# Optimization experiments

Hardware: AMD Instinct MI355X
Metric: run time of the kernel (lower is better)

## Reference

```python
import math
import jax, jax.numpy as jnp
import numpy as np

B, DIN, DOUT = 16384, 512, 512
LATERAL_K = 3
K_WTA = max(1, int(DOUT * 0.25))


def _build_L_mask(dout: int, k: int) -> np.ndarray:
    m = np.zeros((dout, dout), dtype=np.float32)
    for j in range(dout):
        nb = []
        for off in range(1, k + 1):
            if j - off >= 0:
                nb.append(j - off)
            if j + off < dout:
                nb.append(j + off)
        for n in nb[:k]:
            m[j, n] = 1.0
    return m


def _kwta_mask(x):
    # top-k winner-take-all mask along last dim (ties resolved like torch.topk)
    _, idx = jax.lax.top_k(x, K_WTA)
    rows = jnp.arange(x.shape[0])[:, None]
    return jnp.zeros_like(x).at[rows, idx].set(1.0)


def _phi(x, mask):
    return jax.nn.gelu(x, approximate=False) * mask


def _phi_deriv(x, mask):
    cdf = 0.5 * (1.0 + jax.lax.erf(x / math.sqrt(2.0)))
    pdf = jnp.exp(-0.5 * x * x) / math.sqrt(2.0 * math.pi)
    return (cdf + x * pdf) * mask


def _clip_update(d, max_norm):
    n = jnp.linalg.norm(d)  # global norm over the whole tensor, as in torch
    return jnp.where(n > max_norm, d * (max_norm / (n + 1e-8)), d)


def setup_inputs() -> dict:
    key = jax.random.key(0)
    ks = jax.random.split(key, 8)
    k_v = math.sqrt(1.0 / DIN)
    k_w = math.sqrt(1.0 / DOUT)
    return {
        "bottom_up": jax.random.normal(ks[0], (B, DIN), jnp.float32),
        "td_target": jax.random.normal(ks[1], (B, DOUT), jnp.float32) * 0.5,
        "x": jax.random.normal(ks[2], (B, DOUT), jnp.float32) * 0.5,
        "V": jax.random.uniform(ks[3], (DIN, DOUT), jnp.float32, -k_v, k_v),
        "b_in": jnp.full((DOUT,), -5.0, jnp.float32),
        "W_snap": jax.random.uniform(ks[4], (DOUT, DIN), jnp.float32, -k_w, k_w),
        "b_out_snap": jnp.zeros((DIN,), jnp.float32),
        "L": jax.random.uniform(ks[5], (DOUT, DOUT), jnp.float32, -0.1, 0.1),
        "L_mask": jnp.asarray(_build_L_mask(DOUT, LATERAL_K)),
        "step_i": 2,
    }


def reference(bottom_up, td_target, x, V, b_in, W_snap, b_out_snap, L, L_mask, step_i):
    tau, eta_x, lambda_act = 0.5, 0.8, 1e-6
    mask = _kwta_mask(x)
    phi_x = _phi(x, mask)                                     # [B, DOUT]
    prediction = phi_x @ W_snap + b_out_snap                  # [B, DIN]
    error = jax.lax.stop_gradient(bottom_up - prediction)     # detached in torch
    feedback_drive = (error @ W_snap.T) * _phi_deriv(x, mask)
    forward_drive = bottom_up @ V + b_in                      # [B, DOUT]
    recognition_drive = forward_drive - x                     # recognition_weight=1.0
    top_down_drive = 3.0 * (td_target - x)
    lateral_drive = phi_x @ (L * L_mask)
    state_grad = (feedback_drive + recognition_drive + top_down_drive
                  + 0.3 * lateral_drive - lambda_act * jnp.sign(x))
    eta = eta_x / (1.0 + 0.1 * step_i)
    dx = _clip_update(tau * eta * state_grad, 1.0)
    return jnp.clip(x + dx, -5.0, 5.0)
```

## Files before the change

kernel.cpp:

```cpp
#include <hip/hip_runtime.h>
#include <hip/hip_bf16.h>
#include <cstdint>


#define DEV static __device__ __forceinline__

typedef __attribute__((ext_vector_type(8))) short short8;
typedef __attribute__((ext_vector_type(4))) float f32x4;

static constexpr int BATCH = 16384;
static constexpr int D = 512;

DEV unsigned short f2bf(float f) {
  unsigned u = __float_as_uint(f);
  return (unsigned short)((u + 0x7FFFu + ((u >> 16) & 1u)) >> 16);
}
DEV float bf2f(unsigned short h) { return __uint_as_float(((unsigned)h) << 16); }

DEV float wsumf(float v) { for (int o = 32; o; o >>= 1) v += __shfl_xor(v, o, 64); return v; }

DEV void gload16(const void* g, void* l) {
  __builtin_amdgcn_global_load_lds((const __attribute__((address_space(1))) void*)g,
                                   (__attribute__((address_space(3))) void*)l, 16, 0, 0);
}

DEV void load8(const float* rowp, int lane, float v[8]) {
  const float4* q = (const float4*)rowp;
  float4 a = q[lane * 2], b = q[lane * 2 + 1];
  v[0] = a.x; v[1] = a.y; v[2] = a.z; v[3] = a.w;
  v[4] = b.x; v[5] = b.y; v[6] = b.z; v[7] = b.w;
}

__global__ __launch_bounds__(256) void prep_k(
    const float* __restrict__ W, const float* __restrict__ V,
    const float* __restrict__ L, const float* __restrict__ Lm,
    unsigned short* __restrict__ Wbt, unsigned short* __restrict__ Wb2,
    unsigned short* __restrict__ Vbt, float* __restrict__ Mc7,
    float* __restrict__ ssq)
{
  int idx = blockIdx.x * 256 + threadIdx.x;
  int n = idx >> 9, k = idx & 511;
  Wbt[idx] = f2bf(W[k * D + n]);
  Wb2[idx] = f2bf(W[idx]);
  Vbt[idx] = f2bf(V[k * D + n]);
  if (idx < 7 * D) {
    int t = idx >> 9, nn = idx & 511;
    int j = nn - 3 + t;
    float v = 0.f;
    if (j >= 0 && j < D && j != nn) v = L[j * D + nn] * Lm[j * D + nn];
    Mc7[idx] = v;
  }
  if (idx == 0) *ssq = 0.f;
}

__global__ __launch_bounds__(256) void kwta_k(
    const float* __restrict__ x, const float* __restrict__ td,
    const float* __restrict__ bu, const float* __restrict__ b_in,
    const float* __restrict__ Mc7,
    unsigned short* __restrict__ phi16, unsigned short* __restrict__ pd16,
    unsigned short* __restrict__ base16, unsigned short* __restrict__ bu16)
{
  __shared__ float pbuf[4][D];
  const int tid = threadIdx.x, lane = tid & 63, wv = tid >> 6;
  const int row = blockIdx.x * 4 + wv;
  const size_t rbase = (size_t)row * D;

  float xv[8];
  load8(x + rbase, lane, xv);
  unsigned key[8];
  #pragma unroll
  for (int s = 0; s < 8; ++s) {
    unsigned u = __float_as_uint(xv[s]);
    key[s] = (u & 0x80000000u) ? ~u : (u | 0x80000000u);
  }
  unsigned T = 0u;
  for (int bit = 31; bit >= 0; --bit) {
    unsigned cand = T | (1u << bit);
    int c = 0;
    #pragma unroll
    for (int s = 0; s < 8; ++s) c += (int)__popcll(__ballot(key[s] >= cand));
    T = (c >= 128) ? cand : T;
  }
  int cg = 0;
  unsigned long long em[8];
  #pragma unroll
  for (int s = 0; s < 8; ++s) {
    cg += (int)__popcll(__ballot(key[s] > T));
    em[s] = __ballot(key[s] == T);
  }
  const int rneed = 128 - cg;
  const unsigned long long lower = (1ull << lane) - 1ull;
  int run = 0;
  #pragma unroll
  for (int s = 0; s < 8; ++s) run += (int)__popcll(em[s] & lower);

  float phiv[8], pdv[8];
  float* pb = pbuf[wv];
  #pragma unroll
  for (int s = 0; s < 8; ++s) {
    bool sel = key[s] > T;
    if (key[s] == T) { sel = (run < rneed); ++run; }
    float v = xv[s];
    float cdf = 0.5f * (1.0f + erff(v * 0.7071067811865476f));
    float ph = sel ? v * cdf : 0.0f;
    float pd = sel ? (cdf + v * 0.3989422804014327f * __expf(-0.5f * v * v)) : 0.0f;
    phiv[s] = ph; pdv[s] = pd;
    pb[(s << 6) | lane] = ph;
  }
  __syncthreads();

  float tdv[8], buv[8];
  load8(td + rbase, lane, tdv);
  load8(bu + rbase, lane, buv);

  float lat[8] = {0.f, 0.f, 0.f, 0.f, 0.f, 0.f, 0.f, 0.f};
  #pragma unroll
  for (int t = 0; t < 7; ++t) {
    const float4* mq = (const float4*)(Mc7 + t * D + lane * 8);
    float4 m0 = mq[0], m1 = mq[1];
    float mm[8] = {m0.x, m0.y, m0.z, m0.w, m1.x, m1.y, m1.z, m1.w};
    #pragma unroll
    for (int s = 0; s < 8; ++s) {
      int j = lane * 8 + s - 3 + t;
      int jc = j < 0 ? 0 : (j > D - 1 ? D - 1 : j);
      lat[s] += mm[s] * pb[((jc & 7) << 6) | (jc >> 3)];
    }
  }

  short8 o_phi, o_pd, o_base, o_bu;
  #pragma unroll
  for (int s = 0; s < 8; ++s) {
    int n = lane * 8 + s;
    float v = xv[s];
    float sgn = (v > 0.f) ? 1.f : ((v < 0.f) ? -1.f : 0.f);
    float bs = b_in[n] + 3.f * tdv[s] - 4.f * v + 0.3f * lat[s] - 1e-6f * sgn;
    o_phi[s] = (short)f2bf(phiv[s]);
    o_pd[s]  = (short)f2bf(pdv[s]);
    o_base[s]= (short)f2bf(bs);
    o_bu[s]  = (short)f2bf(buv[s]);
  }
  *(short8*)(phi16 + rbase + lane * 8) = o_phi;
  *(short8*)(pd16  + rbase + lane * 8) = o_pd;
  *(short8*)(base16+ rbase + lane * 8) = o_base;
  *(short8*)(bu16  + rbase + lane * 8) = o_bu;
}

template<int MODE>
__global__ __launch_bounds__(256) void gemm_k(
    const unsigned short* __restrict__ A,
    const unsigned short* __restrict__ Bt,
    const float* __restrict__ f32b,
    const unsigned short* __restrict__ b16a,
    const unsigned short* __restrict__ b16b,
    unsigned short* __restrict__ out16,
    float* __restrict__ outf,
    float* __restrict__ ssq,
    const int* __restrict__ stepi)
{
  constexpr int K = 512;
  __shared__ __align__(16) unsigned short As[128 * 32];
  __shared__ __align__(16) unsigned short Bs[128 * 32];
  const int tid = threadIdx.x;
  const int lane = tid & 63, w = tid >> 6;
  const int m0 = (blockIdx.x >> 2) * 128, n0 = (blockIdx.x & 3) * 128;
  const int qr = (w >> 1) * 64, qc = (w & 1) * 64;
  const int lr = lane & 15, g = lane >> 4;

  f32x4 acc[4][4];
  #pragma unroll
  for (int m = 0; m < 4; ++m)
    #pragma unroll
    for (int n = 0; n < 4; ++n) acc[m][n] = (f32x4){0.f, 0.f, 0.f, 0.f};

  const unsigned short* Abase = A + (size_t)m0 * K;
  const unsigned short* Bbase = Bt + (size_t)n0 * K;

  for (int kt = 0; kt < K; kt += 32) {
    #pragma unroll
    for (int p = 0; p < 2; ++p) {
      int ch = tid + p * 256;
      int row = ch >> 2, kc = (ch & 3) * 8;
      gload16(Abase + (size_t)row * K + kt + kc, As + (size_t)(w * 64 + p * 256) * 8);
      gload16(Bbase + (size_t)row * K + kt + kc, Bs + (size_t)(w * 64 + p * 256) * 8);
    }
    __syncthreads();
    short8 af[4], bfr[4];
    #pragma unroll
    for (int m = 0; m < 4; ++m) af[m]  = *(const short8*)(As + (qr + 16 * m + lr) * 32 + 8 * g);
    #pragma unroll
    for (int n = 0; n < 4; ++n) bfr[n] = *(const short8*)(Bs + (qc + 16 * n + lr) * 32 + 8 * g);
    #pragma unroll
    for (int m = 0; m < 4; ++m)
      #pragma unroll
      for (int n = 0; n < 4; ++n)
        acc[m][n] = __builtin_amdgcn_mfma_f32_16x16x32_bf16(af[m], bfr[n], acc[m][n], 0, 0, 0);
    __syncthreads();
  }

  float tau_eta = 0.f, lssq = 0.f;
  if constexpr (MODE == 3) tau_eta = 0.5f * 0.8f / (1.0f + 0.1f * (float)stepi[0]);
  #pragma unroll
  for (int m = 0; m < 4; ++m) {
    #pragma unroll
    for (int n = 0; n < 4; ++n) {
      #pragma unroll
      for (int r = 0; r < 4; ++r) {
        int row = m0 + qr + 16 * m + 4 * g + r;
        int col = n0 + qc + 16 * n + lr;
        size_t idx = (size_t)row * D + col;
        float v = acc[m][n][r];
        if constexpr (MODE == 1) {
          out16[idx] = f2bf(bf2f(b16a[idx]) - (v + f32b[col]));
        } else if constexpr (MODE == 2) {
          out16[idx] = f2bf(v * bf2f(b16a[idx]));
        } else {
          float dv = tau_eta * (v + bf2f(b16a[idx]) + bf2f(b16b[idx]));
          outf[idx] = dv;
          lssq += dv * dv;
        }
      }
    }
  }
  if constexpr (MODE == 3) {
    lssq = wsumf(lssq);
    if (lane == 0) atomicAdd(ssq, lssq);
  }
}

__global__ __launch_bounds__(256) void final_k(const float* __restrict__ x,
                                               float* __restrict__ d,
                                               const float* __restrict__ ssq)
{
  float nrm = sqrtf(*ssq);
  float s = nrm > 1.0f ? 1.0f / (nrm + 1e-8f) : 1.0f;
  int i = blockIdx.x * 256 + threadIdx.x;
  const float4* xq = (const float4*)x;
  float4* dq = (float4*)d;
  float4 xv = xq[i], dv = dq[i];
  float4 o;
  o.x = fminf(fmaxf(xv.x + s * dv.x, -5.f), 5.f);
  o.y = fminf(fmaxf(xv.y + s * dv.y, -5.f), 5.f);
  o.z = fminf(fmaxf(xv.z + s * dv.z, -5.f), 5.f);
  o.w = fminf(fmaxf(xv.w + s * dv.w, -5.f), 5.f);
  dq[i] = o;
}

extern "C" void kernel_launch(void* const* d_in, const int* in_sizes, int n_in,
                              void* d_out, int out_size, void* d_ws, size_t ws_size,
                              hipStream_t stream) {
  const float* bu    = (const float*)d_in[0];
  const float* td    = (const float*)d_in[1];
  const float* x     = (const float*)d_in[2];
  const float* V     = (const float*)d_in[3];
  const float* b_in  = (const float*)d_in[4];
  const float* W     = (const float*)d_in[5];
  const float* bout  = (const float*)d_in[6];
  const float* L     = (const float*)d_in[7];
  const float* Lm    = (const float*)d_in[8];
  const int*   stepi = (const int*)d_in[9];
  float* dout = (float*)d_out;

  char* p = (char*)d_ws;
  size_t off = 0;
  auto take = [&](size_t bytes) -> void* {
    void* r = (void*)(p + off);
    off += (bytes + 255) & ~(size_t)255;
    return r;
  };
  float* ssq            = (float*)take(4);
  unsigned short* Wbt   = (unsigned short*)take((size_t)D * D * 2);
  unsigned short* Wb2   = (unsigned short*)take((size_t)D * D * 2);
  unsigned short* Vbt   = (unsigned short*)take((size_t)D * D * 2);
  float* Mc7            = (float*)take((size_t)7 * D * 4);
  const size_t bd = (size_t)BATCH * D * 2;
  unsigned short* phi16 = (unsigned short*)take(bd);
  unsigned short* bu16  = (unsigned short*)take(bd);
  unsigned short* pd16  = (unsigned short*)take(bd);
  unsigned short* bse16 = (unsigned short*)take(bd);
  unsigned short* err16 = (unsigned short*)take(bd);
  unsigned short* fb16  = phi16;

  prep_k<<<(D * D) / 256, 256, 0, stream>>>(W, V, L, Lm, Wbt, Wb2, Vbt, Mc7, ssq);
  kwta_k<<<BATCH / 4, 256, 0, stream>>>(x, td, bu, b_in, Mc7, phi16, pd16, bse16, bu16);
  gemm_k<1><<<(BATCH / 128) * (D / 128), 256, 0, stream>>>(
      phi16, Wbt, bout, bu16, nullptr, err16, nullptr, nullptr, nullptr);
  gemm_k<2><<<(BATCH / 128) * (D / 128), 256, 0, stream>>>(
      err16, Wb2, nullptr, pd16, nullptr, fb16, nullptr, nullptr, nullptr);
  gemm_k<3><<<(BATCH / 128) * (D / 128), 256, 0, stream>>>(
      bu16, Vbt, nullptr, fb16, bse16, nullptr, dout, ssq, stepi);
  final_k<<<(BATCH * D / 4) / 256, 256, 0, stream>>>(x, dout, ssq);
}
```

Measured before the change: 263.4 us.

## Double-buffer GEMM tiles, swizzle blocks, approximate erf, early-exit top-k, bf16 dx

Measured after the change: 278.7 us. 5.8% more time.

```diff
diff --git a/kernel.cpp b/kernel.cpp
--- a/kernel.cpp
+++ b/kernel.cpp
@@ -74,36 +74,56 @@
     key[s] = (u & 0x80000000u) ? ~u : (u | 0x80000000u);
   }
   unsigned T = 0u;
+  bool exact = false;
   for (int bit = 31; bit >= 0; --bit) {
     unsigned cand = T | (1u << bit);
     int c = 0;
     #pragma unroll
     for (int s = 0; s < 8; ++s) c += (int)__popcll(__ballot(key[s] >= cand));
-    T = (c >= 128) ? cand : T;
-  }
-  int cg = 0;
-  unsigned long long em[8];
-  #pragma unroll
-  for (int s = 0; s < 8; ++s) {
-    cg += (int)__popcll(__ballot(key[s] > T));
-    em[s] = __ballot(key[s] == T);
-  }
-  const int rneed = 128 - cg;
-  const unsigned long long lower = (1ull << lane) - 1ull;
-  int run = 0;
-  #pragma unroll
-  for (int s = 0; s < 8; ++s) run += (int)__popcll(em[s] & lower);
+    if (c == 128) { T = cand; exact = true; break; }
+    if (c > 128) T = cand;
+  }
+
+  bool selv[8];
+  if (exact) {
+    #pragma unroll
+    for (int s = 0; s < 8; ++s) selv[s] = (key[s] >= T);
+  } else {
+    int cg = 0;
+    unsigned long long em[8];
+    #pragma unroll
+    for (int s = 0; s < 8; ++s) {
+      cg += (int)__popcll(__ballot(key[s] > T));
+      em[s] = __ballot(key[s] == T);
+    }
+    const int rneed = 128 - cg;
+    const unsigned long long lower = (1ull << lane) - 1ull;
+    int run = 0;
+    #pragma unroll
+    for (int s = 0; s < 8; ++s) run += (int)__popcll(em[s] & lower);
+    #pragma unroll
+    for (int s = 0; s < 8; ++s) {
+      bool sel = key[s] > T;
+      if (key[s] == T) { sel = (run < rneed); ++run; }
+      selv[s] = sel;
+    }
+  }
 
   float phiv[8], pdv[8];
   float* pb = pbuf[wv];
   #pragma unroll
   for (int s = 0; s < 8; ++s) {
-    bool sel = key[s] > T;
-    if (key[s] == T) { sel = (run < rneed); ++run; }
     float v = xv[s];
-    float cdf = 0.5f * (1.0f + erff(v * 0.7071067811865476f));
-    float ph = sel ? v * cdf : 0.0f;
-    float pd = sel ? (cdf + v * 0.3989422804014327f * __expf(-0.5f * v * v)) : 0.0f;
+    float e  = __expf(-0.5f * v * v);
+    float az = fabsf(v) * 0.7071067811865476f;
+    float t  = __builtin_amdgcn_rcpf(1.0f + 0.3275911f * az);
+    float p  = 0.254829592f + t * (-0.284496736f + t * (1.421413741f +
+               t * (-1.453152027f + t * 1.061405429f)));
+    float erfa = 1.0f - p * t * e;
+    float erfs = (v < 0.f) ? -erfa : erfa;
+    float cdf = 0.5f * (1.0f + erfs);
+    float ph = selv[s] ? v * cdf : 0.0f;
+    float pd = selv[s] ? (cdf + v * 0.3989422804014327f * e) : 0.0f;
     phiv[s] = ph; pdv[s] = pd;
     pb[(s << 6) | lane] = ph;
   }
@@ -153,16 +173,17 @@
     const unsigned short* __restrict__ b16a,
     const unsigned short* __restrict__ b16b,
     unsigned short* __restrict__ out16,
-    float* __restrict__ outf,
     float* __restrict__ ssq,
     const int* __restrict__ stepi)
 {
   constexpr int K = 512;
-  __shared__ __align__(16) unsigned short As[128 * 32];
-  __shared__ __align__(16) unsigned short Bs[128 * 32];
+  constexpr int NT = K / 32;
+  __shared__ __align__(16) unsigned short As[2][128 * 32];
+  __shared__ __align__(16) unsigned short Bs[2][128 * 32];
   const int tid = threadIdx.x;
   const int lane = tid & 63, w = tid >> 6;
-  const int m0 = (blockIdx.x >> 2) * 128, n0 = (blockIdx.x & 3) * 128;
+  const int lid = (blockIdx.x & 7) * 64 + (blockIdx.x >> 3);
+  const int m0 = (lid >> 2) * 128, n0 = (lid & 3) * 128;
   const int qr = (w >> 1) * 64, qc = (w & 1) * 64;
   const int lr = lane & 15, g = lane >> 4;
 
@@ -175,20 +196,27 @@
   const unsigned short* Abase = A + (size_t)m0 * K;
   const unsigned short* Bbase = Bt + (size_t)n0 * K;
 
-  for (int kt = 0; kt < K; kt += 32) {
-    #pragma unroll
-    for (int p = 0; p < 2; ++p) {
-      int ch = tid + p * 256;
-      int row = ch >> 2, kc = (ch & 3) * 8;
-      gload16(Abase + (size_t)row * K + kt + kc, As + (size_t)(w * 64 + p * 256) * 8);
-      gload16(Bbase + (size_t)row * K + kt + kc, Bs + (size_t)(w * 64 + p * 256) * 8);
-    }
-    __syncthreads();
+  const int ch0 = tid, ch1 = tid + 256;
+  const int r0 = ch0 >> 2, c0 = (ch0 & 3) * 8;
+  const int r1 = ch1 >> 2, c1 = (ch1 & 3) * 8;
+  auto stage = [&](int buf, int kt) {
+    gload16(Abase + r0 * K + kt + c0, As[buf] + (size_t)(w * 64) * 8);
+    gload16(Bbase + r0 * K + kt + c0, Bs[buf] + (size_t)(w * 64) * 8);
+    gload16(Abase + r1 * K + kt + c1, As[buf] + (size_t)(w * 64 + 256) * 8);
+    gload16(Bbase + r1 * K + kt + c1, Bs[buf] + (size_t)(w * 64 + 256) * 8);
+  };
+
+  stage(0, 0);
+  __syncthreads();
+  #pragma unroll
+  for (int kt = 0; kt < NT; ++kt) {
+    const int cur = kt & 1;
+    if (kt + 1 < NT) stage(cur ^ 1, (kt + 1) * 32);
     short8 af[4], bfr[4];
     #pragma unroll
-    for (int m = 0; m < 4; ++m) af[m]  = *(const short8*)(As + (qr + 16 * m + lr) * 32 + 8 * g);
-    #pragma unroll
-    for (int n = 0; n < 4; ++n) bfr[n] = *(const short8*)(Bs + (qc + 16 * n + lr) * 32 + 8 * g);
+    for (int m = 0; m < 4; ++m) af[m]  = *(const short8*)(As[cur] + (qr + 16 * m + lr) * 32 + 8 * g);
+    #pragma unroll
+    for (int n = 0; n < 4; ++n) bfr[n] = *(const short8*)(Bs[cur] + (qc + 16 * n + lr) * 32 + 8 * g);
     #pragma unroll
     for (int m = 0; m < 4; ++m)
       #pragma unroll
@@ -215,7 +243,7 @@
           out16[idx] = f2bf(v * bf2f(b16a[idx]));
         } else {
           float dv = tau_eta * (v + bf2f(b16a[idx]) + bf2f(b16b[idx]));
-          outf[idx] = dv;
+          out16[idx] = f2bf(dv);
           lssq += dv * dv;
         }
       }
@@ -228,21 +256,27 @@
 }
 
 __global__ __launch_bounds__(256) void final_k(const float* __restrict__ x,
-                                               float* __restrict__ d,
+                                               const unsigned short* __restrict__ d16,
+                                               float* __restrict__ out,
                                                const float* __restrict__ ssq)
 {
   float nrm = sqrtf(*ssq);
   float s = nrm > 1.0f ? 1.0f / (nrm + 1e-8f) : 1.0f;
-  int i = blockIdx.x * 256 + threadIdx.x;
-  const float4* xq = (const float4*)x;
-  float4* dq = (float4*)d;
-  float4 xv = xq[i], dv = dq[i];
-  float4 o;
-  o.x = fminf(fmaxf(xv.x + s * dv.x, -5.f), 5.f);
-  o.y = fminf(fmaxf(xv.y + s * dv.y, -5.f), 5.f);
-  o.z = fminf(fmaxf(xv.z + s * dv.z, -5.f), 5.f);
-  o.w = fminf(fmaxf(xv.w + s * dv.w, -5.f), 5.f);
-  dq[i] = o;
+  size_t i = (size_t)blockIdx.x * 256 + threadIdx.x;
+  short8 dv = *(const short8*)(d16 + i * 8);
+  const float4* xq = (const float4*)(x + i * 8);
+  float4 xa = xq[0], xb = xq[1];
+  float4 oa, ob;
+  oa.x = fminf(fmaxf(xa.x + s * bf2f((unsigned short)dv[0]), -5.f), 5.f);
+  oa.y = fminf(fmaxf(xa.y + s * bf2f((unsigned short)dv[1]), -5.f), 5.f);
+  oa.z = fminf(fmaxf(xa.z + s * bf2f((unsigned short)dv[2]), -5.f), 5.f);
+  oa.w = fminf(fmaxf(xa.w + s * bf2f((unsigned short)dv[3]), -5.f), 5.f);
+  ob.x = fminf(fmaxf(xb.x + s * bf2f((unsigned short)dv[4]), -5.f), 5.f);
+  ob.y = fminf(fmaxf(xb.y + s * bf2f((unsigned short)dv[5]), -5.f), 5.f);
+  ob.z = fminf(fmaxf(xb.z + s * bf2f((unsigned short)dv[6]), -5.f), 5.f);
+  ob.w = fminf(fmaxf(xb.w + s * bf2f((unsigned short)dv[7]), -5.f), 5.f);
+  float4* oq = (float4*)(out + i * 8);
+  oq[0] = oa; oq[1] = ob;
 }
 
 extern "C" void kernel_launch(void* const* d_in, const int* in_sizes, int n_in,
@@ -279,14 +313,15 @@
   unsigned short* bse16 = (unsigned short*)take(bd);
   unsigned short* err16 = (unsigned short*)take(bd);
   unsigned short* fb16  = phi16;
+  unsigned short* d16   = err16;
 
   prep_k<<<(D * D) / 256, 256, 0, stream>>>(W, V, L, Lm, Wbt, Wb2, Vbt, Mc7, ssq);
   kwta_k<<<BATCH / 4, 256, 0, stream>>>(x, td, bu, b_in, Mc7, phi16, pd16, bse16, bu16);
   gemm_k<1><<<(BATCH / 128) * (D / 128), 256, 0, stream>>>(
-      phi16, Wbt, bout, bu16, nullptr, err16, nullptr, nullptr, nullptr);
+      phi16, Wbt, bout, bu16, nullptr, err16, nullptr, nullptr);
   gemm_k<2><<<(BATCH / 128) * (D / 128), 256, 0, stream>>>(
-      err16, Wb2, nullptr, pd16, nullptr, fb16, nullptr, nullptr, nullptr);
+      err16, Wb2, nullptr, pd16, nullptr, fb16, nullptr, nullptr);
   gemm_k<3><<<(BATCH / 128) * (D / 128), 256, 0, stream>>>(
-      bu16, Vbt, nullptr, fb16, bse16, nullptr, dout, ssq, stepi);
-  final_k<<<(BATCH * D / 4) / 256, 256, 0, stream>>>(x, dout, ssq);
-}
+      bu16, Vbt, nullptr, fb16, bse16, d16, ssq, stepi);
+  final_k<<<BATCH * D / 8 / 256, 256, 0, stream>>>(x, d16, dout, ssq);
+}
```
